# Kernel tuning notes

Measured on AMD Instinct MI355X. Metric: run time of the kernel, lower is better.

Reference implementation:

```python
import jax, jax.numpy as jnp
import numpy as np

N_NODES = 100000
N_EDGES = 400000
N_GRAPHS = 4096
IN_DIM = 128
HID = 64
HEADS = 8
NEG_SLOPE = 0.2


def setup_inputs() -> dict:
    key = jax.random.key(0)
    ks = jax.random.split(key, 12)
    x = jax.random.normal(ks[0], (N_NODES, IN_DIM), dtype=jnp.float32)
    edge_index = jax.random.randint(ks[1], (2, N_EDGES), 0, N_NODES, dtype=jnp.int64)
    batch = jnp.sort(jax.random.randint(ks[2], (N_NODES,), 0, N_GRAPHS, dtype=jnp.int64))
    s = 1.0 / np.sqrt(IN_DIM)
    W1 = jax.random.normal(ks[3], (IN_DIM, HEADS * HID), dtype=jnp.float32) * s
    att_src1 = jax.random.normal(ks[4], (HEADS, HID), dtype=jnp.float32) * 0.1
    att_dst1 = jax.random.normal(ks[5], (HEADS, HID), dtype=jnp.float32) * 0.1
    b1 = jnp.zeros((HEADS * HID,), dtype=jnp.float32)
    s2 = 1.0 / np.sqrt(HEADS * HID)
    W2 = jax.random.normal(ks[6], (HEADS * HID, HID), dtype=jnp.float32) * s2
    att_src2 = jax.random.normal(ks[7], (1, HID), dtype=jnp.float32) * 0.1
    att_dst2 = jax.random.normal(ks[8], (1, HID), dtype=jnp.float32) * 0.1
    b2 = jnp.zeros((HID,), dtype=jnp.float32)
    Wf = jax.random.normal(ks[9], (HID, 1), dtype=jnp.float32) * (1.0 / np.sqrt(HID))
    bf = jnp.zeros((1,), dtype=jnp.float32)
    return {"x": x, "edge_index": edge_index, "batch": batch,
            "W1": W1, "att_src1": att_src1, "att_dst1": att_dst1, "b1": b1,
            "W2": W2, "att_src2": att_src2, "att_dst2": att_dst2, "b2": b2,
            "Wf": Wf, "bf": bf}


def _gat_layer(x, src, dst, W, att_src, att_dst, bias, heads, out_ch, concat):
    # PyG GATConv math (add_self_loops handled by caller via src/dst)
    n = x.shape[0]
    h = (x @ W).reshape(n, heads, out_ch)          # [N, H, C]
    a_s = (h * att_src[None]).sum(-1)               # [N, H]
    a_d = (h * att_dst[None]).sum(-1)               # [N, H]
    alpha = a_s[src] + a_d[dst]                     # [E, H]
    alpha = jax.nn.leaky_relu(alpha, NEG_SLOPE)
    amax = jax.ops.segment_max(alpha, dst, num_segments=n)
    alpha = jnp.exp(alpha - amax[dst])
    denom = jax.ops.segment_sum(alpha, dst, num_segments=n)
    alpha = alpha / (denom[dst] + 1e-16)
    msg = h[src] * alpha[:, :, None]                # [E, H, C]
    out = jax.ops.segment_sum(msg, dst, num_segments=n)  # [N, H, C]
    out = out.reshape(n, heads * out_ch) if concat else out.mean(axis=1)
    return out + bias


def reference(x, edge_index, batch, W1, att_src1, att_dst1, b1,
              W2, att_src2, att_dst2, b2, Wf, bf):
    n = x.shape[0]
    loop = jnp.arange(n, dtype=edge_index.dtype)
    src = jnp.concatenate([edge_index[0], loop])
    dst = jnp.concatenate([edge_index[1], loop])
    h = _gat_layer(x, src, dst, W1, att_src1, att_dst1, b1, HEADS, HID, True)
    h = jax.nn.relu(h)
    h = _gat_layer(h, src, dst, W2, att_src2, att_dst2, b2, 1, HID, False)
    h = jax.nn.relu(h)
    sums = jax.ops.segment_sum(h, batch, num_segments=N_GRAPHS)        # [G, HID]
    cnts = jax.ops.segment_sum(jnp.ones((n,), h.dtype), batch, num_segments=N_GRAPHS)
    pooled = sums / jnp.clip(cnts, 1.0)[:, None]
    return pooled @ Wf + bf
```

## Files before the change

### kernel.cpp

```cpp
#include <hip/hip_runtime.h>

typedef short bfrag8 __attribute__((ext_vector_type(8)));
typedef float f32x4 __attribute__((ext_vector_type(4)));
typedef unsigned int uint4v __attribute__((ext_vector_type(4)));

__device__ __forceinline__ unsigned short f2bf(float f) {
    unsigned u = __float_as_uint(f);
    u += 0x7fffu + ((u >> 16) & 1u);
    return (unsigned short)(u >> 16);
}
__device__ __forceinline__ float bf2f(unsigned short s) {
    return __uint_as_float((unsigned)s << 16);
}

__global__ __launch_bounds__(256) void zero_i32(int* __restrict__ p, int n) {
    int i = (int)(blockIdx.x * 256u + threadIdx.x);
    int stride = gridDim.x * 256;
    for (; i < n; i += stride) p[i] = 0;
}

__global__ __launch_bounds__(256) void cvt_f32_bf16(const float* __restrict__ in,
                                                    unsigned short* __restrict__ out, size_t n) {
    size_t i = (blockIdx.x * 256llu + threadIdx.x) * 4;
    size_t stride = (size_t)gridDim.x * 1024llu;
    for (; i < n; i += stride) {
        float4 v = *(const float4*)(in + i);
        out[i + 0] = f2bf(v.x);
        out[i + 1] = f2bf(v.y);
        out[i + 2] = f2bf(v.z);
        out[i + 3] = f2bf(v.w);
    }
}

__global__ __launch_bounds__(256) void prep_w1(const float* __restrict__ W1,
                                               unsigned short* __restrict__ out) {
    int i = (int)(blockIdx.x * 256u + threadIdx.x);
    if (i >= 8 * 4 * 4 * 64 * 8) return;
    int e = i & 7, l = (i >> 3) & 63, c = (i >> 9) & 3, s = (i >> 11) & 3, h = i >> 13;
    int k = s * 32 + (l >> 4) * 8 + e;
    int col = h * 64 + c * 16 + (l & 15);
    out[i] = f2bf(W1[k * 512 + col]);
}

__global__ __launch_bounds__(256) void prep_w2(const float* __restrict__ W2,
                                               unsigned short* __restrict__ out) {
    int i = (int)(blockIdx.x * 256u + threadIdx.x);
    if (i >= 16 * 4 * 64 * 8) return;
    int e = i & 7, l = (i >> 3) & 63, c = (i >> 9) & 3, s = i >> 11;
    int k = s * 32 + (l >> 4) * 8 + e;
    int col = c * 16 + (l & 15);
    out[i] = f2bf(W2[k * 64 + col]);
}

__global__ __launch_bounds__(256) void hist_kernel(const int* __restrict__ ei,
                                                   int* __restrict__ cnt, int E, int N) {
    int t = (int)(blockIdx.x * 256u + threadIdx.x);
    if (t >= E + N) return;
    int dst = (t < E) ? ei[E + t] : t - E;
    atomicAdd(cnt + dst, 1);
}

#define SCAN_BLK 2048
__global__ __launch_bounds__(256) void scan1(const int* __restrict__ cnt,
                                             int* __restrict__ rs,
                                             int* __restrict__ bsum, int N) {
    __shared__ int lds[256];
    int base = blockIdx.x * SCAN_BLK;
    int vals[8];
    int tsum = 0;
    int idx0 = base + threadIdx.x * 8;
#pragma unroll
    for (int j = 0; j < 8; ++j) {
        int i = idx0 + j;
        int v = (i < N) ? cnt[i] : 0;
        vals[j] = tsum;
        tsum += v;
    }
    lds[threadIdx.x] = tsum;
    __syncthreads();
    for (int off = 1; off < 256; off <<= 1) {
        int v = lds[threadIdx.x];
        int u = (threadIdx.x >= (unsigned)off) ? lds[threadIdx.x - off] : 0;
        __syncthreads();
        lds[threadIdx.x] = v + u;
        __syncthreads();
    }
    int texcl = (threadIdx.x == 0) ? 0 : lds[threadIdx.x - 1];
#pragma unroll
    for (int j = 0; j < 8; ++j) {
        int i = idx0 + j;
        if (i < N) rs[i] = texcl + vals[j];
    }
    if (threadIdx.x == 255) bsum[blockIdx.x] = lds[255];
}

__global__ void scan2(int* __restrict__ bsum, int* __restrict__ rs, int nb, int N) {
    if (threadIdx.x == 0 && blockIdx.x == 0) {
        int run = 0;
        for (int b = 0; b < nb; ++b) { int t = bsum[b]; bsum[b] = run; run += t; }
        rs[N] = run;
    }
}

__global__ __launch_bounds__(256) void scan3(int* __restrict__ rs,
                                             const int* __restrict__ bsum, int N) {
    int i = (int)(blockIdx.x * 256u + threadIdx.x);
    if (i < N) rs[i] += bsum[i / SCAN_BLK];
}

__global__ __launch_bounds__(256) void scatter_kernel(const int* __restrict__ ei,
                                                      const int* __restrict__ rs,
                                                      int* __restrict__ cur,
                                                      int* __restrict__ csrc, int E, int N) {
    int t = (int)(blockIdx.x * 256u + threadIdx.x);
    if (t >= E + N) return;
    int src, dst;
    if (t < E) { src = ei[t]; dst = ei[E + t]; } else { src = dst = t - E; }
    int pos = rs[dst] + atomicAdd(cur + dst, 1);
    csrc[pos] = src;
}

__global__ __launch_bounds__(256) void gstart_build(const int* __restrict__ batch,
                                                    int* __restrict__ gstart, int N, int G) {
    int i = (int)(blockIdx.x * 256u + threadIdx.x);
    if (i > N) return;
    if (i == N) {
        int p = batch[N - 1];
        for (int g = p + 1; g <= G; ++g) gstart[g] = N;
    } else {
        int b = batch[i];
        int p = (i == 0) ? -1 : batch[i - 1];
        for (int g = p + 1; g <= b; ++g) gstart[g] = i;
    }
}

__global__ __launch_bounds__(256) void gemm_l1(const unsigned short* __restrict__ A,
                                               const unsigned short* __restrict__ Bfrag,
                                               unsigned short* __restrict__ Cbf,
                                               int M, int ldc, int asStride,
                                               const float* __restrict__ avs,
                                               const float* __restrict__ avd,
                                               float* __restrict__ as_,
                                               float* __restrict__ ad_) {
    const int lane = threadIdx.x & 63;
    const int wave = threadIdx.x >> 6;
    const int l15 = lane & 15, l16 = lane >> 4;
    const int cb = blockIdx.y;
    const long rowBase = (long)blockIdx.x * 128 + wave * 32;

    bfrag8 bf[4][4];
    const bfrag8* bp = (const bfrag8*)(Bfrag + (size_t)cb * 8192);
#pragma unroll
    for (int s = 0; s < 4; ++s)
#pragma unroll
        for (int c = 0; c < 4; ++c)
            bf[s][c] = bp[(s * 4 + c) * 64 + lane];

    f32x4 acc[2][4];
#pragma unroll
    for (int r = 0; r < 2; ++r)
#pragma unroll
        for (int c = 0; c < 4; ++c)
#pragma unroll
            for (int e = 0; e < 4; ++e) acc[r][c][e] = 0.f;

    long r0 = rowBase + l15;        if (r0 > M - 1) r0 = M - 1;
    long r1 = rowBase + 16 + l15;   if (r1 > M - 1) r1 = M - 1;
    const unsigned short* a0p = A + r0 * 128 + l16 * 8;
    const unsigned short* a1p = A + r1 * 128 + l16 * 8;

#pragma unroll
    for (int s = 0; s < 4; ++s) {
        bfrag8 a0 = *(const bfrag8*)(a0p + s * 32);
        bfrag8 a1 = *(const bfrag8*)(a1p + s * 32);
#pragma unroll
        for (int c = 0; c < 4; ++c) {
            acc[0][c] = __builtin_amdgcn_mfma_f32_16x16x32_bf16(a0, bf[s][c], acc[0][c], 0, 0, 0);
            acc[1][c] = __builtin_amdgcn_mfma_f32_16x16x32_bf16(a1, bf[s][c], acc[1][c], 0, 0, 0);
        }
    }

    float avsv[4], avdv[4];
#pragma unroll
    for (int c = 0; c < 4; ++c) {
        avsv[c] = avs[cb * 64 + c * 16 + l15];
        avdv[c] = avd[cb * 64 + c * 16 + l15];
    }

#pragma unroll
    for (int r = 0; r < 2; ++r) {
#pragma unroll
        for (int reg = 0; reg < 4; ++reg) {
            long row = rowBase + r * 16 + l16 * 4 + reg;
            bool ok = row < M;
            float ps = 0.f, pd = 0.f;
#pragma unroll
            for (int c = 0; c < 4; ++c) {
                float v = acc[r][c][reg];
                if (ok) Cbf[row * ldc + cb * 64 + c * 16 + l15] = f2bf(v);
                ps += v * avsv[c];
                pd += v * avdv[c];
            }
#pragma unroll
            for (int off = 1; off < 16; off <<= 1) {
                ps += __shfl_xor(ps, off);
                pd += __shfl_xor(pd, off);
            }
            if (l15 == 0 && ok) {
                as_[row * asStride + cb] = ps;
                ad_[row * asStride + cb] = pd;
            }
        }
    }
}

__global__ __launch_bounds__(256) void gemm_l2_k512(const unsigned short* __restrict__ A,
                                                    const unsigned short* __restrict__ Bfrag,
                                                    unsigned short* __restrict__ Cbf,
                                                    int M,
                                                    const float* __restrict__ avs,
                                                    const float* __restrict__ avd,
                                                    float* __restrict__ as_,
                                                    float* __restrict__ ad_) {
    const int lane = threadIdx.x & 63;
    const int wave = threadIdx.x >> 6;
    const int l15 = lane & 15, l16 = lane >> 4;
    const long rowBase = (long)blockIdx.x * 128 + wave * 32;
    const bfrag8* bp = (const bfrag8*)Bfrag;

    f32x4 acc[2][4];
#pragma unroll
    for (int r = 0; r < 2; ++r)
#pragma unroll
        for (int c = 0; c < 4; ++c)
#pragma unroll
            for (int e = 0; e < 4; ++e) acc[r][c][e] = 0.f;

    long r0 = rowBase + l15;        if (r0 > M - 1) r0 = M - 1;
    long r1 = rowBase + 16 + l15;   if (r1 > M - 1) r1 = M - 1;
    const unsigned short* a0p = A + r0 * 512 + l16 * 8;
    const unsigned short* a1p = A + r1 * 512 + l16 * 8;

    for (int s = 0; s < 16; ++s) {
        bfrag8 a0 = *(const bfrag8*)(a0p + s * 32);
        bfrag8 a1 = *(const bfrag8*)(a1p + s * 32);
        bfrag8 bf0 = bp[(s * 4 + 0) * 64 + lane];
        bfrag8 bf1 = bp[(s * 4 + 1) * 64 + lane];
        bfrag8 bf2 = bp[(s * 4 + 2) * 64 + lane];
        bfrag8 bf3 = bp[(s * 4 + 3) * 64 + lane];
        acc[0][0] = __builtin_amdgcn_mfma_f32_16x16x32_bf16(a0, bf0, acc[0][0], 0, 0, 0);
        acc[1][0] = __builtin_amdgcn_mfma_f32_16x16x32_bf16(a1, bf0, acc[1][0], 0, 0, 0);
        acc[0][1] = __builtin_amdgcn_mfma_f32_16x16x32_bf16(a0, bf1, acc[0][1], 0, 0, 0);
        acc[1][1] = __builtin_amdgcn_mfma_f32_16x16x32_bf16(a1, bf1, acc[1][1], 0, 0, 0);
        acc[0][2] = __builtin_amdgcn_mfma_f32_16x16x32_bf16(a0, bf2, acc[0][2], 0, 0, 0);
        acc[1][2] = __builtin_amdgcn_mfma_f32_16x16x32_bf16(a1, bf2, acc[1][2], 0, 0, 0);
        acc[0][3] = __builtin_amdgcn_mfma_f32_16x16x32_bf16(a0, bf3, acc[0][3], 0, 0, 0);
        acc[1][3] = __builtin_amdgcn_mfma_f32_16x16x32_bf16(a1, bf3, acc[1][3], 0, 0, 0);
    }

    float avsv[4], avdv[4];
#pragma unroll
    for (int c = 0; c < 4; ++c) {
        avsv[c] = avs[c * 16 + l15];
        avdv[c] = avd[c * 16 + l15];
    }

#pragma unroll
    for (int r = 0; r < 2; ++r) {
#pragma unroll
        for (int reg = 0; reg < 4; ++reg) {
            long row = rowBase + r * 16 + l16 * 4 + reg;
            bool ok = row < M;
            float ps = 0.f, pd = 0.f;
#pragma unroll
            for (int c = 0; c < 4; ++c) {
                float v = acc[r][c][reg];
                if (ok) Cbf[row * 64 + c * 16 + l15] = f2bf(v);
                ps += v * avsv[c];
                pd += v * avdv[c];
            }
#pragma unroll
            for (int off = 1; off < 16; off <<= 1) {
                ps += __shfl_xor(ps, off);
                pd += __shfl_xor(pd, off);
            }
            if (l15 == 0 && ok) { as_[row] = ps; ad_[row] = pd; }
        }
    }
}

template<bool ACC, bool WF32, bool WBF16, bool ATTN>
__global__ __launch_bounds__(256) void gemm_acc(const unsigned short* __restrict__ A,
                                                const unsigned short* __restrict__ Bfrag,
                                                float* __restrict__ Cf32,
                                                unsigned short* __restrict__ Cbf,
                                                int M,
                                                const float* __restrict__ avs,
                                                const float* __restrict__ avd,
                                                float* __restrict__ as_,
                                                float* __restrict__ ad_) {
    const int lane = threadIdx.x & 63;
    const int wave = threadIdx.x >> 6;
    const int l15 = lane & 15, l16 = lane >> 4;
    const long rowBase = (long)blockIdx.x * 128 + wave * 32;

    bfrag8 bf[2][4];
    const bfrag8* bp = (const bfrag8*)Bfrag;
#pragma unroll
    for (int s = 0; s < 2; ++s)
#pragma unroll
        for (int c = 0; c < 4; ++c)
            bf[s][c] = bp[(s * 4 + c) * 64 + lane];

    f32x4 acc[2][4];
#pragma unroll
    for (int r = 0; r < 2; ++r)
#pragma unroll
        for (int c = 0; c < 4; ++c)
#pragma unroll
            for (int e = 0; e < 4; ++e) acc[r][c][e] = 0.f;

    long r0 = rowBase + l15;        if (r0 > M - 1) r0 = M - 1;
    long r1 = rowBase + 16 + l15;   if (r1 > M - 1) r1 = M - 1;
    const unsigned short* a0p = A + r0 * 64 + l16 * 8;
    const unsigned short* a1p = A + r1 * 64 + l16 * 8;

#pragma unroll
    for (int s = 0; s < 2; ++s) {
        bfrag8 a0 = *(const bfrag8*)(a0p + s * 32);
        bfrag8 a1 = *(const bfrag8*)(a1p + s * 32);
#pragma unroll
        for (int c = 0; c < 4; ++c) {
            acc[0][c] = __builtin_amdgcn_mfma_f32_16x16x32_bf16(a0, bf[s][c], acc[0][c], 0, 0, 0);
            acc[1][c] = __builtin_amdgcn_mfma_f32_16x16x32_bf16(a1, bf[s][c], acc[1][c], 0, 0, 0);
        }
    }

    float avsv[4], avdv[4];
    if (ATTN) {
#pragma unroll
        for (int c = 0; c < 4; ++c) {
            avsv[c] = avs[c * 16 + l15];
            avdv[c] = avd[c * 16 + l15];
        }
    }

#pragma unroll
    for (int r = 0; r < 2; ++r) {
#pragma unroll
        for (int reg = 0; reg < 4; ++reg) {
            long row = rowBase + r * 16 + l16 * 4 + reg;
            bool ok = row < M;
            float ps = 0.f, pd = 0.f;
#pragma unroll
            for (int c = 0; c < 4; ++c) {
                float v = acc[r][c][reg];
                long idx = row * 64 + c * 16 + l15;
                if (ACC && ok) v += Cf32[idx];
                if (WF32 && ok) Cf32[idx] = v;
                if (WBF16 && ok) Cbf[idx] = f2bf(v);
                if (ATTN) { ps += v * avsv[c]; pd += v * avdv[c]; }
            }
            if (ATTN) {
#pragma unroll
                for (int off = 1; off < 16; off <<= 1) {
                    ps += __shfl_xor(ps, off);
                    pd += __shfl_xor(pd, off);
                }
                if (l15 == 0 && ok) { as_[row] = ps; ad_[row] = pd; }
            }
        }
    }
}

__global__ __launch_bounds__(256) void gather8(const int* __restrict__ csrc,
                                               const int* __restrict__ rs,
                                               const float* __restrict__ as_,
                                               const float* __restrict__ ad_,
                                               const unsigned short* __restrict__ h,
                                               const float* __restrict__ bias,
                                               unsigned short* __restrict__ outp,
                                               int N) {
    int node = (int)((blockIdx.x * 256u + threadIdx.x) >> 6);
    int lane = threadIdx.x & 63;
    if (node >= N) return;
    int myh = lane >> 3;
    int s0 = rs[node], s1 = rs[node + 1];
    float adn = ad_[(size_t)node * 8 + myh];
    float den = 0.f;
    float2 acc[4] = {};
    const unsigned* hu = (const unsigned*)h;
    int k = s0;
    for (; k + 4 <= s1; k += 4) {
        int i0 = csrc[k], i1 = csrc[k + 1], i2 = csrc[k + 2], i3 = csrc[k + 3];
        float a0 = as_[(size_t)i0 * 8 + myh] + adn;
        float a1 = as_[(size_t)i1 * 8 + myh] + adn;
        float a2 = as_[(size_t)i2 * 8 + myh] + adn;
        float a3 = as_[(size_t)i3 * 8 + myh] + adn;
        a0 = a0 > 0.f ? a0 : 0.2f * a0;  a1 = a1 > 0.f ? a1 : 0.2f * a1;
        a2 = a2 > 0.f ? a2 : 0.2f * a2;  a3 = a3 > 0.f ? a3 : 0.2f * a3;
        float w0 = __expf(fminf(a0, 60.f)), w1 = __expf(fminf(a1, 60.f));
        float w2 = __expf(fminf(a2, 60.f)), w3 = __expf(fminf(a3, 60.f));
        uint4v v0 = *(const uint4v*)(hu + (size_t)i0 * 256 + lane * 4);
        uint4v v1 = *(const uint4v*)(hu + (size_t)i1 * 256 + lane * 4);
        uint4v v2 = *(const uint4v*)(hu + (size_t)i2 * 256 + lane * 4);
        uint4v v3 = *(const uint4v*)(hu + (size_t)i3 * 256 + lane * 4);
        den += (w0 + w1) + (w2 + w3);
#pragma unroll
        for (int j = 0; j < 4; ++j) {
            acc[j].x += w0 * __uint_as_float(v0[j] << 16);
            acc[j].y += w0 * __uint_as_float(v0[j] & 0xffff0000u);
            acc[j].x += w1 * __uint_as_float(v1[j] << 16);
            acc[j].y += w1 * __uint_as_float(v1[j] & 0xffff0000u);
            acc[j].x += w2 * __uint_as_float(v2[j] << 16);
            acc[j].y += w2 * __uint_as_float(v2[j] & 0xffff0000u);
            acc[j].x += w3 * __uint_as_float(v3[j] << 16);
            acc[j].y += w3 * __uint_as_float(v3[j] & 0xffff0000u);
        }
    }
    for (; k < s1; ++k) {
        int i0 = csrc[k];
        float a = as_[(size_t)i0 * 8 + myh] + adn;
        a = a > 0.f ? a : 0.2f * a;
        float w = __expf(fminf(a, 60.f));
        uint4v v0 = *(const uint4v*)(hu + (size_t)i0 * 256 + lane * 4);
        den += w;
#pragma unroll
        for (int j = 0; j < 4; ++j) {
            acc[j].x += w * __uint_as_float(v0[j] << 16);
            acc[j].y += w * __uint_as_float(v0[j] & 0xffff0000u);
        }
    }
    float rden = 1.f / (den + 1e-16f);
    uint4v o;
#pragma unroll
    for (int j = 0; j < 4; ++j) {
        float vlo = acc[j].x * rden + bias[lane * 8 + 2 * j];
        float vhi = acc[j].y * rden + bias[lane * 8 + 2 * j + 1];
        vlo = vlo > 0.f ? vlo : 0.f;
        vhi = vhi > 0.f ? vhi : 0.f;
        o[j] = (unsigned)f2bf(vlo) | ((unsigned)f2bf(vhi) << 16);
    }
    __builtin_nontemporal_store(o, (uint4v*)(outp + (size_t)node * 512 + lane * 8));
}

template<bool OBF>
__global__ __launch_bounds__(256) void gather1(const int* __restrict__ csrc,
                                               const int* __restrict__ rs,
                                               const float* __restrict__ as_,
                                               const float* __restrict__ ad_,
                                               const unsigned short* __restrict__ h,
                                               const float* __restrict__ bias,
                                               void* __restrict__ outp, int N) {
    int node = (int)((blockIdx.x * 256u + threadIdx.x) >> 6);
    int lane = threadIdx.x & 63;
    if (node >= N) return;
    int s0 = rs[node], s1 = rs[node + 1];
    float adn = ad_[node];
    float den = 0.f, acc = 0.f;
    int k = s0;
    for (; k + 4 <= s1; k += 4) {
        int i0 = csrc[k], i1 = csrc[k + 1], i2 = csrc[k + 2], i3 = csrc[k + 3];
        float a0 = as_[i0] + adn, a1 = as_[i1] + adn, a2 = as_[i2] + adn, a3 = as_[i3] + adn;
        a0 = a0 > 0.f ? a0 : 0.2f * a0;  a1 = a1 > 0.f ? a1 : 0.2f * a1;
        a2 = a2 > 0.f ? a2 : 0.2f * a2;  a3 = a3 > 0.f ? a3 : 0.2f * a3;
        float w0 = __expf(fminf(a0, 60.f)), w1 = __expf(fminf(a1, 60.f));
        float w2 = __expf(fminf(a2, 60.f)), w3 = __expf(fminf(a3, 60.f));
        float h0 = bf2f(h[(size_t)i0 * 64 + lane]);
        float h1 = bf2f(h[(size_t)i1 * 64 + lane]);
        float h2 = bf2f(h[(size_t)i2 * 64 + lane]);
        float h3 = bf2f(h[(size_t)i3 * 64 + lane]);
        den += (w0 + w1) + (w2 + w3);
        acc += w0 * h0;  acc += w1 * h1;  acc += w2 * h2;  acc += w3 * h3;
    }
    for (; k < s1; ++k) {
        int i0 = csrc[k];
        float a = as_[i0] + adn;
        a = a > 0.f ? a : 0.2f * a;
        float w = __expf(fminf(a, 60.f));
        den += w;
        acc += w * bf2f(h[(size_t)i0 * 64 + lane]);
    }
    float v = acc / (den + 1e-16f) + bias[lane];
    v = v > 0.f ? v : 0.f;
    if (OBF) ((unsigned short*)outp)[(size_t)node * 64 + lane] = f2bf(v);
    else     ((float*)outp)[(size_t)node * 64 + lane] = v;
}

__global__ __launch_bounds__(256) void pool_readout(const float* __restrict__ h2,
                                                    const int* __restrict__ gstart,
                                                    const float* __restrict__ Wf,
                                                    const float* __restrict__ bf,
                                                    float* __restrict__ out, int G) {
    int g = (int)((blockIdx.x * 256u + threadIdx.x) >> 6);
    int lane = threadIdx.x & 63;
    if (g >= G) return;
    int s0 = gstart[g], s1 = gstart[g + 1];
    float acc = 0.f;
    int i = s0;
    for (; i + 2 <= s1; i += 2) {
        acc += h2[(size_t)i * 64 + lane];
        acc += h2[(size_t)(i + 1) * 64 + lane];
    }
    if (i < s1) acc += h2[(size_t)i * 64 + lane];
    float c = (float)(s1 - s0);
    c = c < 1.f ? 1.f : c;
    float v = acc / c * Wf[lane];
#pragma unroll
    for (int off = 32; off; off >>= 1) v += __shfl_xor(v, off);
    if (lane == 0) out[g] = v + bf[0];
}

extern "C" void kernel_launch(void* const* d_in, const int* in_sizes, int n_in,
                              void* d_out, int out_size, void* d_ws, size_t ws_size,
                              hipStream_t stream) {
    const float* x        = (const float*)d_in[0];
    const int*   ei       = (const int*)d_in[1];
    const int*   batch    = (const int*)d_in[2];
    const float* W1       = (const float*)d_in[3];
    const float* att_src1 = (const float*)d_in[4];
    const float* att_dst1 = (const float*)d_in[5];
    const float* b1       = (const float*)d_in[6];
    const float* W2       = (const float*)d_in[7];
    const float* att_src2 = (const float*)d_in[8];
    const float* att_dst2 = (const float*)d_in[9];
    const float* b2       = (const float*)d_in[10];
    const float* Wf       = (const float*)d_in[11];
    const float* bf       = (const float*)d_in[12];
    float* out = (float*)d_out;

    const int N = in_sizes[2];
    const int E = in_sizes[1] / 2;
    const int G = out_size;

    const int nb = (N + SCAN_BLK - 1) / SCAN_BLK;
    const int nodeWaveGrid = (int)(((size_t)N * 64 + 255) / 256);
    const int edgeGrid = (E + N + 255) / 256;
    const int gemmGrid = (N + 127) / 128;

    char* base = (char*)d_ws;
    size_t off = 0;
    auto alloc = [&](size_t bytes) { char* p = base + off; off += (bytes + 255) & ~255llu; return p; };
    unsigned short* wf1   = (unsigned short*)alloc(131072);
    unsigned short* wf2   = (unsigned short*)alloc(65536);
    float* as1            = (float*)alloc((size_t)N * 8 * 4);
    float* ad1            = (float*)alloc((size_t)N * 8 * 4);
    int*   cnt_i          = (int*)alloc((size_t)N * 4);
    int*   rs             = (int*)alloc((size_t)(N + 1) * 4);
    int*   csrc           = (int*)alloc((size_t)(E + N) * 4);
    int*   bsum           = (int*)alloc(1024);
    int*   gstart         = (int*)alloc((size_t)(G + 1) * 4);
    unsigned short* x_bf  = (unsigned short*)alloc((size_t)N * 128 * 2);
    float* ob2            = (float*)x_bf;
    unsigned short* h2bf  = (unsigned short*)alloc((size_t)N * 64 * 2);
    size_t commonEnd = off;

    size_t fusedNeed = commonEnd + 2 * (((size_t)N * 512 * 2 + 255) & ~255llu);
    bool fused = ws_size >= fusedNeed;

    cvt_f32_bf16<<<2048, 256, 0, stream>>>(x, x_bf, (size_t)N * 128);
    prep_w1<<<(8 * 4 * 4 * 64 * 8) / 256, 256, 0, stream>>>(W1, wf1);
    prep_w2<<<(16 * 4 * 64 * 8) / 256, 256, 0, stream>>>(W2, wf2);

    zero_i32<<<512, 256, 0, stream>>>(cnt_i, N);
    hist_kernel<<<edgeGrid, 256, 0, stream>>>(ei, cnt_i, E, N);
    scan1<<<nb, 256, 0, stream>>>(cnt_i, rs, bsum, N);
    scan2<<<1, 1, 0, stream>>>(bsum, rs, nb, N);
    scan3<<<(N + 255) / 256, 256, 0, stream>>>(rs, bsum, N);
    zero_i32<<<512, 256, 0, stream>>>(cnt_i, N);
    scatter_kernel<<<edgeGrid, 256, 0, stream>>>(ei, rs, cnt_i, csrc, E, N);
    gstart_build<<<(N + 256) / 256, 256, 0, stream>>>(batch, gstart, N, G);

    if (fused) {
        unsigned short* h1_bf  = (unsigned short*)alloc((size_t)N * 512 * 2);
        unsigned short* ob1_bf = (unsigned short*)alloc((size_t)N * 512 * 2);

        dim3 g1(gemmGrid, 8);
        gemm_l1<<<g1, 256, 0, stream>>>(x_bf, wf1, h1_bf, N, 512, 8,
                                        att_src1, att_dst1, as1, ad1);
        gather8<<<nodeWaveGrid, 256, 0, stream>>>(csrc, rs, as1, ad1, h1_bf, b1, ob1_bf, N);

        gemm_l2_k512<<<gemmGrid, 256, 0, stream>>>(ob1_bf, wf2, h2bf, N,
                                                   att_src2, att_dst2, as1, ad1);
        gather1<false><<<nodeWaveGrid, 256, 0, stream>>>(csrc, rs, as1, ad1, h2bf, b2, ob2, N);
    } else {
        unsigned short* hb_bf = (unsigned short*)alloc((size_t)N * 64 * 2);
        unsigned short* ob_bf = (unsigned short*)alloc((size_t)N * 64 * 2);
        float* h2acc          = (float*)alloc((size_t)N * 64 * 4);

        for (int h = 0; h < 8; ++h) {
            dim3 g1(gemmGrid, 1);
            gemm_l1<<<g1, 256, 0, stream>>>(x_bf, wf1 + (size_t)h * 8192, hb_bf, N, 64, 1,
                                            att_src1 + h * 64, att_dst1 + h * 64, as1, ad1);
            gather1<true><<<nodeWaveGrid, 256, 0, stream>>>(csrc, rs, as1, ad1, hb_bf, b1 + h * 64, ob_bf, N);
            if (h == 0) {
                gemm_acc<false, true, false, false><<<gemmGrid, 256, 0, stream>>>(
                    ob_bf, wf2, h2acc, nullptr, N, nullptr, nullptr, nullptr, nullptr);
            } else if (h < 7) {
                gemm_acc<true, true, false, false><<<gemmGrid, 256, 0, stream>>>(
                    ob_bf, wf2 + (size_t)h * 4096, h2acc, nullptr, N, nullptr, nullptr, nullptr, nullptr);
            } else {
                gemm_acc<true, false, true, true><<<gemmGrid, 256, 0, stream>>>(
                    ob_bf, wf2 + (size_t)h * 4096, h2acc, h2bf, N,
                    att_src2, att_dst2, as1, ad1);
            }
        }
        gather1<false><<<nodeWaveGrid, 256, 0, stream>>>(csrc, rs, as1, ad1, h2bf, b2, ob2, N);
    }

    pool_readout<<<(G * 64 + 255) / 256, 256, 0, stream>>>(ob2, gstart, Wf, bf, out, G);
}
```

Baseline: 314.9 us.

## Fuse layer-1 attention gather with layer-2 GEMM through LDS

Merges the 8-head aggregation kernel and the K=512 layer-2 GEMM into one kernel. Each block gathers 64 nodes into a swizzled 64KB LDS tile, then runs MFMA against W2 and writes h2 plus the layer-2 attention scores. This removes the write and re-read of the N×512 bf16 intermediate and one launch. The cost is 64KB of LDS per block, which limits occupancy for the latency-bound gather phase, and the GEMM now runs one 16-row tile per wave. Separate as2/ad2 buffers are added so layer-2 scores no longer overwrite the layer-1 ones.

```diff
diff --git a/kernel.cpp b/kernel.cpp
--- a/kernel.cpp
+++ b/kernel.cpp
@@ -210,81 +210,6 @@
                 as_[row * asStride + cb] = ps;
                 ad_[row * asStride + cb] = pd;
             }
-        }
-    }
-}
-
-__global__ __launch_bounds__(256) void gemm_l2_k512(const unsigned short* __restrict__ A,
-                                                    const unsigned short* __restrict__ Bfrag,
-                                                    unsigned short* __restrict__ Cbf,
-                                                    int M,
-                                                    const float* __restrict__ avs,
-                                                    const float* __restrict__ avd,
-                                                    float* __restrict__ as_,
-                                                    float* __restrict__ ad_) {
-    const int lane = threadIdx.x & 63;
-    const int wave = threadIdx.x >> 6;
-    const int l15 = lane & 15, l16 = lane >> 4;
-    const long rowBase = (long)blockIdx.x * 128 + wave * 32;
-    const bfrag8* bp = (const bfrag8*)Bfrag;
-
-    f32x4 acc[2][4];
-#pragma unroll
-    for (int r = 0; r < 2; ++r)
-#pragma unroll
-        for (int c = 0; c < 4; ++c)
-#pragma unroll
-            for (int e = 0; e < 4; ++e) acc[r][c][e] = 0.f;
-
-    long r0 = rowBase + l15;        if (r0 > M - 1) r0 = M - 1;
-    long r1 = rowBase + 16 + l15;   if (r1 > M - 1) r1 = M - 1;
-    const unsigned short* a0p = A + r0 * 512 + l16 * 8;
-    const unsigned short* a1p = A + r1 * 512 + l16 * 8;
-
-    for (int s = 0; s < 16; ++s) {
-        bfrag8 a0 = *(const bfrag8*)(a0p + s * 32);
-        bfrag8 a1 = *(const bfrag8*)(a1p + s * 32);
-        bfrag8 bf0 = bp[(s * 4 + 0) * 64 + lane];
-        bfrag8 bf1 = bp[(s * 4 + 1) * 64 + lane];
-        bfrag8 bf2 = bp[(s * 4 + 2) * 64 + lane];
-        bfrag8 bf3 = bp[(s * 4 + 3) * 64 + lane];
-        acc[0][0] = __builtin_amdgcn_mfma_f32_16x16x32_bf16(a0, bf0, acc[0][0], 0, 0, 0);
-        acc[1][0] = __builtin_amdgcn_mfma_f32_16x16x32_bf16(a1, bf0, acc[1][0], 0, 0, 0);
-        acc[0][1] = __builtin_amdgcn_mfma_f32_16x16x32_bf16(a0, bf1, acc[0][1], 0, 0, 0);
-        acc[1][1] = __builtin_amdgcn_mfma_f32_16x16x32_bf16(a1, bf1, acc[1][1], 0, 0, 0);
-        acc[0][2] = __builtin_amdgcn_mfma_f32_16x16x32_bf16(a0, bf2, acc[0][2], 0, 0, 0);
-        acc[1][2] = __builtin_amdgcn_mfma_f32_16x16x32_bf16(a1, bf2, acc[1][2], 0, 0, 0);
-        acc[0][3] = __builtin_amdgcn_mfma_f32_16x16x32_bf16(a0, bf3, acc[0][3], 0, 0, 0);
-        acc[1][3] = __builtin_amdgcn_mfma_f32_16x16x32_bf16(a1, bf3, acc[1][3], 0, 0, 0);
-    }
-
-    float avsv[4], avdv[4];
-#pragma unroll
-    for (int c = 0; c < 4; ++c) {
-        avsv[c] = avs[c * 16 + l15];
-        avdv[c] = avd[c * 16 + l15];
-    }
-
-#pragma unroll
-    for (int r = 0; r < 2; ++r) {
-#pragma unroll
-        for (int reg = 0; reg < 4; ++reg) {
-            long row = rowBase + r * 16 + l16 * 4 + reg;
-            bool ok = row < M;
-            float ps = 0.f, pd = 0.f;
-#pragma unroll
-            for (int c = 0; c < 4; ++c) {
-                float v = acc[r][c][reg];
-                if (ok) Cbf[row * 64 + c * 16 + l15] = f2bf(v);
-                ps += v * avsv[c];
-                pd += v * avdv[c];
-            }
-#pragma unroll
-            for (int off = 1; off < 16; off <<= 1) {
-                ps += __shfl_xor(ps, off);
-                pd += __shfl_xor(pd, off);
-            }
-            if (l15 == 0 && ok) { as_[row] = ps; ad_[row] = pd; }
         }
     }
 }
@@ -373,75 +298,139 @@
     }
 }
 
-__global__ __launch_bounds__(256) void gather8(const int* __restrict__ csrc,
-                                               const int* __restrict__ rs,
-                                               const float* __restrict__ as_,
-                                               const float* __restrict__ ad_,
-                                               const unsigned short* __restrict__ h,
-                                               const float* __restrict__ bias,
-                                               unsigned short* __restrict__ outp,
-                                               int N) {
-    int node = (int)((blockIdx.x * 256u + threadIdx.x) >> 6);
-    int lane = threadIdx.x & 63;
-    if (node >= N) return;
-    int myh = lane >> 3;
-    int s0 = rs[node], s1 = rs[node + 1];
-    float adn = ad_[(size_t)node * 8 + myh];
-    float den = 0.f;
-    float2 acc[4] = {};
+__global__ __launch_bounds__(256) void gat_fused(const int* __restrict__ csrc,
+                                                 const int* __restrict__ rs,
+                                                 const float* __restrict__ as_,
+                                                 const float* __restrict__ ad_,
+                                                 const unsigned short* __restrict__ h,
+                                                 const float* __restrict__ bias,
+                                                 const unsigned short* __restrict__ Bfrag,
+                                                 unsigned short* __restrict__ h2bf,
+                                                 const float* __restrict__ avs,
+                                                 const float* __restrict__ avd,
+                                                 float* __restrict__ as2,
+                                                 float* __restrict__ ad2, int N) {
+    __shared__ unsigned char ldsb[64 * 1024];
+    const int tid = threadIdx.x;
+    const int lane = tid & 63;
+    const int wave = tid >> 6;
     const unsigned* hu = (const unsigned*)h;
-    int k = s0;
-    for (; k + 4 <= s1; k += 4) {
-        int i0 = csrc[k], i1 = csrc[k + 1], i2 = csrc[k + 2], i3 = csrc[k + 3];
-        float a0 = as_[(size_t)i0 * 8 + myh] + adn;
-        float a1 = as_[(size_t)i1 * 8 + myh] + adn;
-        float a2 = as_[(size_t)i2 * 8 + myh] + adn;
-        float a3 = as_[(size_t)i3 * 8 + myh] + adn;
-        a0 = a0 > 0.f ? a0 : 0.2f * a0;  a1 = a1 > 0.f ? a1 : 0.2f * a1;
-        a2 = a2 > 0.f ? a2 : 0.2f * a2;  a3 = a3 > 0.f ? a3 : 0.2f * a3;
-        float w0 = __expf(fminf(a0, 60.f)), w1 = __expf(fminf(a1, 60.f));
-        float w2 = __expf(fminf(a2, 60.f)), w3 = __expf(fminf(a3, 60.f));
-        uint4v v0 = *(const uint4v*)(hu + (size_t)i0 * 256 + lane * 4);
-        uint4v v1 = *(const uint4v*)(hu + (size_t)i1 * 256 + lane * 4);
-        uint4v v2 = *(const uint4v*)(hu + (size_t)i2 * 256 + lane * 4);
-        uint4v v3 = *(const uint4v*)(hu + (size_t)i3 * 256 + lane * 4);
-        den += (w0 + w1) + (w2 + w3);
-#pragma unroll
-        for (int j = 0; j < 4; ++j) {
-            acc[j].x += w0 * __uint_as_float(v0[j] << 16);
-            acc[j].y += w0 * __uint_as_float(v0[j] & 0xffff0000u);
-            acc[j].x += w1 * __uint_as_float(v1[j] << 16);
-            acc[j].y += w1 * __uint_as_float(v1[j] & 0xffff0000u);
-            acc[j].x += w2 * __uint_as_float(v2[j] << 16);
-            acc[j].y += w2 * __uint_as_float(v2[j] & 0xffff0000u);
-            acc[j].x += w3 * __uint_as_float(v3[j] << 16);
-            acc[j].y += w3 * __uint_as_float(v3[j] & 0xffff0000u);
-        }
-    }
-    for (; k < s1; ++k) {
-        int i0 = csrc[k];
-        float a = as_[(size_t)i0 * 8 + myh] + adn;
-        a = a > 0.f ? a : 0.2f * a;
-        float w = __expf(fminf(a, 60.f));
-        uint4v v0 = *(const uint4v*)(hu + (size_t)i0 * 256 + lane * 4);
-        den += w;
-#pragma unroll
-        for (int j = 0; j < 4; ++j) {
-            acc[j].x += w * __uint_as_float(v0[j] << 16);
-            acc[j].y += w * __uint_as_float(v0[j] & 0xffff0000u);
-        }
-    }
-    float rden = 1.f / (den + 1e-16f);
-    uint4v o;
-#pragma unroll
-    for (int j = 0; j < 4; ++j) {
-        float vlo = acc[j].x * rden + bias[lane * 8 + 2 * j];
-        float vhi = acc[j].y * rden + bias[lane * 8 + 2 * j + 1];
-        vlo = vlo > 0.f ? vlo : 0.f;
-        vhi = vhi > 0.f ? vhi : 0.f;
-        o[j] = (unsigned)f2bf(vlo) | ((unsigned)f2bf(vhi) << 16);
-    }
-    __builtin_nontemporal_store(o, (uint4v*)(outp + (size_t)node * 512 + lane * 8));
+
+    for (int t = wave; t < 64; t += 4) {
+        int node = blockIdx.x * 64 + t;
+        uint4v o = {0u, 0u, 0u, 0u};
+        if (node < N) {
+            int myh = lane >> 3;
+            int s0 = rs[node], s1 = rs[node + 1];
+            float adn = ad_[(size_t)node * 8 + myh];
+            float den = 0.f;
+            float2 acc[4] = {};
+            int k = s0;
+            for (; k + 4 <= s1; k += 4) {
+                int i0 = csrc[k], i1 = csrc[k + 1], i2 = csrc[k + 2], i3 = csrc[k + 3];
+                float a0 = as_[(size_t)i0 * 8 + myh] + adn;
+                float a1 = as_[(size_t)i1 * 8 + myh] + adn;
+                float a2 = as_[(size_t)i2 * 8 + myh] + adn;
+                float a3 = as_[(size_t)i3 * 8 + myh] + adn;
+                a0 = a0 > 0.f ? a0 : 0.2f * a0;  a1 = a1 > 0.f ? a1 : 0.2f * a1;
+                a2 = a2 > 0.f ? a2 : 0.2f * a2;  a3 = a3 > 0.f ? a3 : 0.2f * a3;
+                float w0 = __expf(fminf(a0, 60.f)), w1 = __expf(fminf(a1, 60.f));
+                float w2 = __expf(fminf(a2, 60.f)), w3 = __expf(fminf(a3, 60.f));
+                uint4v v0 = *(const uint4v*)(hu + (size_t)i0 * 256 + lane * 4);
+                uint4v v1 = *(const uint4v*)(hu + (size_t)i1 * 256 + lane * 4);
+                uint4v v2 = *(const uint4v*)(hu + (size_t)i2 * 256 + lane * 4);
+                uint4v v3 = *(const uint4v*)(hu + (size_t)i3 * 256 + lane * 4);
+                den += (w0 + w1) + (w2 + w3);
+#pragma unroll
+                for (int j = 0; j < 4; ++j) {
+                    acc[j].x += w0 * __uint_as_float(v0[j] << 16);
+                    acc[j].y += w0 * __uint_as_float(v0[j] & 0xffff0000u);
+                    acc[j].x += w1 * __uint_as_float(v1[j] << 16);
+                    acc[j].y += w1 * __uint_as_float(v1[j] & 0xffff0000u);
+                    acc[j].x += w2 * __uint_as_float(v2[j] << 16);
+                    acc[j].y += w2 * __uint_as_float(v2[j] & 0xffff0000u);
+                    acc[j].x += w3 * __uint_as_float(v3[j] << 16);
+                    acc[j].y += w3 * __uint_as_float(v3[j] & 0xffff0000u);
+                }
+            }
+            for (; k < s1; ++k) {
+                int i0 = csrc[k];
+                float a = as_[(size_t)i0 * 8 + myh] + adn;
+                a = a > 0.f ? a : 0.2f * a;
+                float w = __expf(fminf(a, 60.f));
+                uint4v v0 = *(const uint4v*)(hu + (size_t)i0 * 256 + lane * 4);
+                den += w;
+#pragma unroll
+                for (int j = 0; j < 4; ++j) {
+                    acc[j].x += w * __uint_as_float(v0[j] << 16);
+                    acc[j].y += w * __uint_as_float(v0[j] & 0xffff0000u);
+                }
+            }
+            float rden = 1.f / (den + 1e-16f);
+#pragma unroll
+            for (int j = 0; j < 4; ++j) {
+                float vlo = acc[j].x * rden + bias[lane * 8 + 2 * j];
+                float vhi = acc[j].y * rden + bias[lane * 8 + 2 * j + 1];
+                vlo = vlo > 0.f ? vlo : 0.f;
+                vhi = vhi > 0.f ? vhi : 0.f;
+                o[j] = (unsigned)f2bf(vlo) | ((unsigned)f2bf(vhi) << 16);
+            }
+        }
+        unsigned byteoff = (unsigned)t * 1024u + (((unsigned)lane * 16u) ^ (((unsigned)(t & 7)) << 4));
+        *(uint4v*)(ldsb + byteoff) = o;
+    }
+    __syncthreads();
+
+    const int l15 = lane & 15, l16 = lane >> 4;
+    const bfrag8* bp = (const bfrag8*)Bfrag;
+    const int rloc = wave * 16 + l15;
+
+    f32x4 acc[4];
+#pragma unroll
+    for (int c = 0; c < 4; ++c)
+#pragma unroll
+        for (int e = 0; e < 4; ++e) acc[c][e] = 0.f;
+
+    for (int s = 0; s < 16; ++s) {
+        unsigned aoff = (unsigned)rloc * 1024u +
+                        (((unsigned)(s * 64 + l16 * 16)) ^ (((unsigned)(rloc & 7)) << 4));
+        bfrag8 a = *(const bfrag8*)(ldsb + aoff);
+        bfrag8 b0 = bp[(s * 4 + 0) * 64 + lane];
+        bfrag8 b1 = bp[(s * 4 + 1) * 64 + lane];
+        bfrag8 b2 = bp[(s * 4 + 2) * 64 + lane];
+        bfrag8 b3 = bp[(s * 4 + 3) * 64 + lane];
+        acc[0] = __builtin_amdgcn_mfma_f32_16x16x32_bf16(a, b0, acc[0], 0, 0, 0);
+        acc[1] = __builtin_amdgcn_mfma_f32_16x16x32_bf16(a, b1, acc[1], 0, 0, 0);
+        acc[2] = __builtin_amdgcn_mfma_f32_16x16x32_bf16(a, b2, acc[2], 0, 0, 0);
+        acc[3] = __builtin_amdgcn_mfma_f32_16x16x32_bf16(a, b3, acc[3], 0, 0, 0);
+    }
+
+    float avsv[4], avdv[4];
+#pragma unroll
+    for (int c = 0; c < 4; ++c) {
+        avsv[c] = avs[c * 16 + l15];
+        avdv[c] = avd[c * 16 + l15];
+    }
+
+#pragma unroll
+    for (int reg = 0; reg < 4; ++reg) {
+        long row = (long)blockIdx.x * 64 + wave * 16 + l16 * 4 + reg;
+        bool ok = row < N;
+        float ps = 0.f, pd = 0.f;
+#pragma unroll
+        for (int c = 0; c < 4; ++c) {
+            float v = acc[c][reg];
+            if (ok) h2bf[row * 64 + c * 16 + l15] = f2bf(v);
+            ps += v * avsv[c];
+            pd += v * avdv[c];
+        }
+#pragma unroll
+        for (int off = 1; off < 16; off <<= 1) {
+            ps += __shfl_xor(ps, off);
+            pd += __shfl_xor(pd, off);
+        }
+        if (l15 == 0 && ok) { as2[row] = ps; ad2[row] = pd; }
+    }
 }
 
 template<bool OBF>
@@ -545,6 +534,8 @@
     unsigned short* wf2   = (unsigned short*)alloc(65536);
     float* as1            = (float*)alloc((size_t)N * 8 * 4);
     float* ad1            = (float*)alloc((size_t)N * 8 * 4);
+    float* as2            = (float*)alloc((size_t)N * 4);
+    float* ad2            = (float*)alloc((size_t)N * 4);
     int*   cnt_i          = (int*)alloc((size_t)N * 4);
     int*   rs             = (int*)alloc((size_t)(N + 1) * 4);
     int*   csrc           = (int*)alloc((size_t)(E + N) * 4);
@@ -555,7 +546,7 @@
     unsigned short* h2bf  = (unsigned short*)alloc((size_t)N * 64 * 2);
     size_t commonEnd = off;
 
-    size_t fusedNeed = commonEnd + 2 * (((size_t)N * 512 * 2 + 255) & ~255llu);
+    size_t fusedNeed = commonEnd + (((size_t)N * 512 * 2 + 255) & ~255llu);
     bool fused = ws_size >= fusedNeed;
 
     cvt_f32_bf16<<<2048, 256, 0, stream>>>(x, x_bf, (size_t)N * 128);
@@ -572,17 +563,15 @@
     gstart_build<<<(N + 256) / 256, 256, 0, stream>>>(batch, gstart, N, G);
 
     if (fused) {
-        unsigned short* h1_bf  = (unsigned short*)alloc((size_t)N * 512 * 2);
-        unsigned short* ob1_bf = (unsigned short*)alloc((size_t)N * 512 * 2);
+        unsigned short* h1_bf = (unsigned short*)alloc((size_t)N * 512 * 2);
 
         dim3 g1(gemmGrid, 8);
         gemm_l1<<<g1, 256, 0, stream>>>(x_bf, wf1, h1_bf, N, 512, 8,
                                         att_src1, att_dst1, as1, ad1);
-        gather8<<<nodeWaveGrid, 256, 0, stream>>>(csrc, rs, as1, ad1, h1_bf, b1, ob1_bf, N);
-
-        gemm_l2_k512<<<gemmGrid, 256, 0, stream>>>(ob1_bf, wf2, h2bf, N,
-                                                   att_src2, att_dst2, as1, ad1);
-        gather1<false><<<nodeWaveGrid, 256, 0, stream>>>(csrc, rs, as1, ad1, h2bf, b2, ob2, N);
+        gat_fused<<<(N + 63) / 64, 256, 0, stream>>>(csrc, rs, as1, ad1, h1_bf, b1,
+                                                     wf2, h2bf, att_src2, att_dst2,
+                                                     as2, ad2, N);
+        gather1<false><<<nodeWaveGrid, 256, 0, stream>>>(csrc, rs, as2, ad2, h2bf, b2, ob2, N);
     } else {
         unsigned short* hb_bf = (unsigned short*)alloc((size_t)N * 64 * 2);
         unsigned short* ob_bf = (unsigned short*)alloc((size_t)N * 64 * 2);
@@ -602,10 +591,10 @@
             } else {
                 gemm_acc<true, false, true, true><<<gemmGrid, 256, 0, stream>>>(
                     ob_bf, wf2 + (size_t)h * 4096, h2acc, h2bf, N,
-                    att_src2, att_dst2, as1, ad1);
-            }
-        }
-        gather1<false><<<nodeWaveGrid, 256, 0, stream>>>(csrc, rs, as1, ad1, h2bf, b2, ob2, N);
+                    att_src2, att_dst2, as2, ad2);
+            }
+        }
+        gather1<false><<<nodeWaveGrid, 256, 0, stream>>>(csrc, rs, as2, ad2, h2bf, b2, ob2, N);
     }
 
     pool_readout<<<(G * 64 + 255) / 256, 256, 0, stream>>>(ob2, gstart, Wf, bf, out, G);
```

Measured after the change: 364.3 us. +15.7%, slower.
